# Performance work log

Hardware: AMD Instinct MI355X
Metric: run time of the kernel (lower is better)

The kernel has to match this reference:

```python
import jax, jax.numpy as jnp
import numpy as np


def setup_inputs() -> dict:
    key = jax.random.key(0)
    k1, k2, k3 = jax.random.split(key, 3)
    B, S_enc, S_dec, D = 8, 4096, 4096, 128
    b = jax.random.normal(k1, (B, S_enc, D), dtype=jnp.float32)
    h = jax.random.normal(k2, (B, S_dec, D), dtype=jnp.float32)
    W_b = jax.random.normal(k3, (D, D), dtype=jnp.float32) * (1.0 / np.sqrt(D))
    return {"b": b, "h": h, "W_b": W_b}


def reference(b, h, W_b):
    # tmp1 = h @ W_b : [B, S_dec, D]
    tmp1 = jnp.einsum('btd,de->bte', h, W_b)
    # scores = tmp1 @ b^T : [B, S_dec, S_enc]
    scores = jnp.einsum('bte,bse->bts', tmp1, b)
    attn = jax.nn.softmax(scores, axis=-1)
    # weighted sum over encoder positions (the original does this via a huge
    # tile/broadcast/multiply/reduce_sum; math is a batched matmul)
    cxt = jnp.einsum('bts,bsd->btd', attn, b)
    return cxt
```

## Files before the change

kernel.cpp:

```cpp
#include <hip/hip_runtime.h>

typedef _Float16 half2v __attribute__((ext_vector_type(2)));
typedef _Float16 half4 __attribute__((ext_vector_type(4)));
typedef _Float16 half8 __attribute__((ext_vector_type(8)));
typedef float floatx4 __attribute__((ext_vector_type(4)));

#define B_   8
#define SE   4096
#define SD   4096
#define D_   128
#define NT   64
#define LDB  136
#define LOG2E 1.44269504f

__device__ __forceinline__ void cp16_async(const _Float16* g, _Float16* l) {
    __builtin_amdgcn_global_load_lds((const __attribute__((address_space(1))) unsigned int*)g,
                                     (__attribute__((address_space(3))) unsigned int*)l, 16, 0, 0);
}

__device__ __forceinline__ float dot2acc(half2v a, half2v b, float c) {
#if __has_builtin(__builtin_amdgcn_fdot2)
    return __builtin_amdgcn_fdot2(a, b, c, false);
#else
    return c + (float)a[0] * (float)b[0] + (float)a[1] * (float)b[1];
#endif
}

__global__ __launch_bounds__(256) void wprep(const float* __restrict__ W,
                                             _Float16* __restrict__ W16,
                                             _Float16* __restrict__ Wlo) {
    int i = blockIdx.x * 256 + threadIdx.x;
    float w = W[i];
    _Float16 hi = (_Float16)w;
    W16[i] = hi;
    Wlo[i] = (_Float16)(w - (float)hi);
}

__global__ __launch_bounds__(256) void kvprep(const float* __restrict__ b,
                                              const _Float16* __restrict__ W16,
                                              const _Float16* __restrict__ Wlo,
                                              _Float16* __restrict__ kp,
                                              _Float16* __restrict__ vT) {
    __shared__ _Float16 bs[64 * LDB];
    const int bb = blockIdx.y, s0 = blockIdx.x * 64;
    const int tid = threadIdx.x, wave = tid >> 6, lane = tid & 63;
    const int l15 = lane & 15, quad = lane >> 4;

    const float* bg = b + ((size_t)bb * SE + s0) * D_;
    #pragma unroll
    for (int it = 0; it < 4; ++it) {
        int idx = tid + it * 256;
        int row = idx >> 4, seg = idx & 15;
        const float* src = bg + row * D_ + seg * 8;
        float4 a = *(const float4*)src;
        float4 c = *(const float4*)(src + 4);
        half8 hv;
        hv[0] = (_Float16)a.x; hv[1] = (_Float16)a.y; hv[2] = (_Float16)a.z; hv[3] = (_Float16)a.w;
        hv[4] = (_Float16)c.x; hv[5] = (_Float16)c.y; hv[6] = (_Float16)c.z; hv[7] = (_Float16)c.w;
        *(half8*)(bs + row * LDB + seg * 8) = hv;
    }
    __syncthreads();

    half8 af[4];
    #pragma unroll
    for (int ks = 0; ks < 4; ++ks)
        af[ks] = *(const half8*)(bs + (wave * 16 + l15) * LDB + ks * 32 + quad * 8);
    floatx4 acc[8];
    #pragma unroll
    for (int nt = 0; nt < 8; ++nt) acc[nt] = (floatx4){0.f, 0.f, 0.f, 0.f};
    #pragma unroll
    for (int ks = 0; ks < 4; ++ks) {
        #pragma unroll
        for (int nt = 0; nt < 8; ++nt) {
            half8 bh = *(const half8*)(W16 + (size_t)(nt * 16 + l15) * 128 + ks * 32 + quad * 8);
            half8 bl = *(const half8*)(Wlo + (size_t)(nt * 16 + l15) * 128 + ks * 32 + quad * 8);
            acc[nt] = __builtin_amdgcn_mfma_f32_16x16x32_f16(af[ks], bh, acc[nt], 0, 0, 0);
            acc[nt] = __builtin_amdgcn_mfma_f32_16x16x32_f16(af[ks], bl, acc[nt], 0, 0, 0);
        }
    }

    {
        const int sq = tid & 15, dg = tid >> 4;
        half8 rowv[4];
        #pragma unroll
        for (int j = 0; j < 4; ++j)
            rowv[j] = *(const half8*)(bs + (sq * 4 + j) * LDB + dg * 8);
        #pragma unroll
        for (int r = 0; r < 8; ++r) {
            int d = dg * 8 + r;
            half4 o;
            #pragma unroll
            for (int j = 0; j < 4; ++j) o[j] = rowv[j][r];
            *(half4*)(vT + ((size_t)bb * D_ + d) * SE + s0 + sq * 4) = o;
        }
    }
    __syncthreads();

    #pragma unroll
    for (int nt = 0; nt < 8; ++nt)
        #pragma unroll
        for (int r = 0; r < 4; ++r)
            bs[(wave * 16 + quad * 4 + r) * LDB + nt * 16 + l15] = (_Float16)acc[nt][r];
    __syncthreads();
    _Float16* kg = kp + ((size_t)bb * SE + s0) * D_;
    {
        const int row = tid >> 2;
        #pragma unroll
        for (int it = 0; it < 4; ++it) {
            int ch = (tid & 3) + it * 4;
            half8 v = *(const half8*)(bs + row * LDB + ch * 8);
            *(half8*)(kg + row * D_ + ch * 8) = v;
        }
    }
}

__global__ __launch_bounds__(512, 4) void flash(const float* __restrict__ h,
                                                const _Float16* __restrict__ k,
                                                const _Float16* __restrict__ vT,
                                                float* __restrict__ out) {
    __shared__ _Float16 KV[2][16384];

    const int bb   = blockIdx.y;
    const int q0   = blockIdx.x * 64;
    const int tid  = threadIdx.x;
    const int wave = tid >> 6;
    const int wq   = wave >> 1;
    const int ws   = wave & 1;
    const int lane = tid & 63;
    const int l15  = lane & 15;
    const int quad = lane >> 4;

    const _Float16* kbase = k + (size_t)bb * SE * D_;
    const _Float16* vbase = vT + (size_t)bb * D_ * SE;

    int koff[2], voff[2];
    #pragma unroll
    for (int it = 0; it < 2; ++it) {
        int i = it * 512 + wave * 64 + lane;
        int kr = i >> 4, kpp = i & 15;
        int km = kr & 15;
        int srow = (kr & 32) + ((km >> 2) << 3) + (((kr >> 4) & 1) << 2) + (km & 3);
        koff[it] = srow * D_ + ((kpp ^ km) * 8);
        int vr = i >> 3, vpp = i & 7;
        voff[it] = vr * SE + ((vpp ^ (vr & 7)) * 8);
    }

    const _Float16* kA0[4]; const _Float16* kA1[4];
    const _Float16 *vB0, *vB1;
    #pragma unroll
    for (int ks = 0; ks < 4; ++ks) {
        int o = l15 * 128 + (((ks * 4 + quad) ^ l15) * 8) + ws * 4096;
        kA0[ks] = &KV[0][o]; kA1[ks] = &KV[1][o];
    }
    {
        int o = 8192 + l15 * 64 + (((ws * 4 + quad) ^ (l15 & 7)) * 8);
        vB0 = &KV[0][o]; vB1 = &KV[1][o];
    }

    {
        _Float16* buf0 = &KV[0][0];
        #pragma unroll
        for (int it = 0; it < 2; ++it) {
            cp16_async(kbase + koff[it], buf0 + (it * 512 + wave * 64) * 8);
            cp16_async(vbase + voff[it], buf0 + 8192 + (it * 512 + wave * 64) * 8);
        }
    }

    half8 qf[4];
    {
        const float* hrow = h + ((size_t)bb * SD + q0 + wq * 16 + l15) * D_;
        #pragma unroll
        for (int ks = 0; ks < 4; ++ks) {
            float4 a = *(const float4*)(hrow + ks * 32 + quad * 8);
            float4 c = *(const float4*)(hrow + ks * 32 + quad * 8 + 4);
            half8 f;
            f[0] = (_Float16)(a.x * LOG2E); f[1] = (_Float16)(a.y * LOG2E);
            f[2] = (_Float16)(a.z * LOG2E); f[3] = (_Float16)(a.w * LOG2E);
            f[4] = (_Float16)(c.x * LOG2E); f[5] = (_Float16)(c.y * LOG2E);
            f[6] = (_Float16)(c.z * LOG2E); f[7] = (_Float16)(c.w * LOG2E);
            qf[ks] = f;
        }
    }

    floatx4 acc_o[8];
    #pragma unroll
    for (int dt = 0; dt < 8; ++dt) acc_o[dt] = (floatx4){0.f, 0.f, 0.f, 0.f};
    float nm = 0.f;
    float l_part = 0.f;
    const half2v one2 = { (_Float16)1.f, (_Float16)1.f };

#define STEP(T, KA, VBP, NBUF)                                                        \
  {                                                                                   \
    __syncthreads();                  \
    if ((T) + 1 < SE / NT) {                                                          \
      const _Float16* kt = kbase + (size_t)((T) + 1) * (NT * D_);                     \
      const _Float16* vt = vbase + (size_t)((T) + 1) * NT;                            \
      _Float16* bufn = (NBUF);                                                        \
      _Pragma("unroll")                                                               \
      for (int it = 0; it < 2; ++it) {                                                \
        cp16_async(kt + koff[it], bufn + (it * 512 + wave * 64) * 8);                 \
        cp16_async(vt + voff[it], bufn + 8192 + (it * 512 + wave * 64) * 8);          \
      }                                                                               \
    }                                                                                 \
                        \
    floatx4 accs[2];                                                                  \
    accs[0] = (floatx4){nm, nm, nm, nm};                                              \
    accs[1] = accs[0];                                                                \
    _Pragma("unroll")                                                                 \
    for (int ks = 0; ks < 4; ++ks) {                                                  \
      half8 af0 = *(const half8*)(KA[ks]);                                            \
      half8 af1 = *(const half8*)(KA[ks] + 2048);                                     \
      accs[0] = __builtin_amdgcn_mfma_f32_16x16x32_f16(af0, qf[ks], accs[0], 0, 0, 0);\
      accs[1] = __builtin_amdgcn_mfma_f32_16x16x32_f16(af1, qf[ks], accs[1], 0, 0, 0);\
    }                                                                                 \
                                     \
    float x0 = fmaxf(fmaxf(accs[0][0], accs[0][1]), accs[0][2]);                      \
    float x1 = fmaxf(fmaxf(accs[0][3], accs[1][0]), accs[1][1]);                      \
    float x2 = fmaxf(fmaxf(accs[1][2], accs[1][3]), x0);                              \
    float mv = fmaxf(x1, x2);                                                         \
    if (__ballot(mv > 11.5f) != 0ull) {              \
      float mr = fmaxf(mv, __shfl_xor(mv, 16, 64));                                   \
      mr = fmaxf(mr, __shfl_xor(mr, 32, 64));                                         \
      float delta = fmaxf(mr, 0.f);                                                   \
      float alpha = exp2f(-delta);                                                    \
      l_part *= alpha;                                                                \
      float ab[4];                                                                    \
      _Pragma("unroll")                                                               \
      for (int r = 0; r < 4; ++r) ab[r] = __shfl(alpha, quad * 4 + r, 64);            \
      _Pragma("unroll")                                                               \
      for (int dt = 0; dt < 8; ++dt)                                                  \
        _Pragma("unroll")                                                             \
        for (int r = 0; r < 4; ++r) acc_o[dt][r] *= ab[r];                            \
      _Pragma("unroll")                                                               \
      for (int stl = 0; stl < 2; ++stl)                                               \
        _Pragma("unroll")                                                             \
        for (int r = 0; r < 4; ++r) accs[stl][r] -= delta;                            \
      nm -= delta;                                                                    \
    }                                                                                 \
         \
    float p0 = exp2f(accs[0][0]), p1 = exp2f(accs[0][1]);                             \
    float p2 = exp2f(accs[0][2]), p3 = exp2f(accs[0][3]);                             \
    float p4 = exp2f(accs[1][0]), p5 = exp2f(accs[1][1]);                             \
    float p6 = exp2f(accs[1][2]), p7 = exp2f(accs[1][3]);                             \
    half2v c0 = __builtin_bit_cast(half2v, __builtin_amdgcn_cvt_pkrtz(p0, p1));       \
    half2v c1 = __builtin_bit_cast(half2v, __builtin_amdgcn_cvt_pkrtz(p2, p3));       \
    half2v c2 = __builtin_bit_cast(half2v, __builtin_amdgcn_cvt_pkrtz(p4, p5));       \
    half2v c3 = __builtin_bit_cast(half2v, __builtin_amdgcn_cvt_pkrtz(p6, p7));       \
    l_part = dot2acc(c0, one2, l_part);                                               \
    l_part = dot2acc(c1, one2, l_part);                                               \
    l_part = dot2acc(c2, one2, l_part);                                               \
    l_part = dot2acc(c3, one2, l_part);                                               \
    half8 pA;                                                                         \
    pA[0] = c0[0]; pA[1] = c0[1]; pA[2] = c1[0]; pA[3] = c1[1];                       \
    pA[4] = c2[0]; pA[5] = c2[1]; pA[6] = c3[0]; pA[7] = c3[1];                       \
         \
    _Pragma("unroll")                                                                 \
    for (int dt = 0; dt < 8; ++dt) {                                                  \
      half8 vf = *(const half8*)((VBP) + dt * 1024);                                  \
      acc_o[dt] = __builtin_amdgcn_mfma_f32_16x16x32_f16(pA, vf, acc_o[dt], 0, 0, 0); \
    }                                                                                 \
  }

    for (int t = 0; t < SE / NT; t += 2) {
        STEP(t,     kA0, vB0, &KV[1][0]);
        STEP(t + 1, kA1, vB1, &KV[0][0]);
    }
#undef STEP

    const float m_q = -nm;
    float l_own;
    {
        float l = l_part;
        l += __shfl_xor(l, 16, 64);
        l += __shfl_xor(l, 32, 64);
        l_own = l;
    }

    __syncthreads();
    float* Ob = (float*)&KV[0][0];
    float* ml = (float*)&KV[1][0];

    if (ws == 1) {
        #pragma unroll
        for (int dt = 0; dt < 8; ++dt)
            *(floatx4*)(Ob + ((wq * 8 + dt) * 64 + lane) * 4) = acc_o[dt];
        if (quad == 0)
            *(float2*)(ml + (wq * 16 + l15) * 2) = make_float2(m_q, l_own);
    }
    __syncthreads();
    if (ws == 0) {
        float m0r[4], l0r[4], m1r[4], l1r[4];
        #pragma unroll
        for (int r = 0; r < 4; ++r) {
            m0r[r] = __shfl(m_q, quad * 4 + r, 64);
            l0r[r] = __shfl(l_own, quad * 4 + r, 64);
            float2 p = *(float2*)(ml + (wq * 16 + quad * 4 + r) * 2);
            m1r[r] = p.x; l1r[r] = p.y;
        }
        float a0[4], a1[4], inv[4];
        #pragma unroll
        for (int r = 0; r < 4; ++r) {
            float mm = fmaxf(m0r[r], m1r[r]);
            a0[r] = exp2f(m0r[r] - mm);
            a1[r] = exp2f(m1r[r] - mm);
            inv[r] = 1.f / (l0r[r] * a0[r] + l1r[r] * a1[r]);
        }
        float* orow = out + ((size_t)bb * SD + q0 + wq * 16 + quad * 4) * D_;
        #pragma unroll
        for (int dt = 0; dt < 8; ++dt) {
            floatx4 o1 = *(floatx4*)(Ob + ((wq * 8 + dt) * 64 + lane) * 4);
            #pragma unroll
            for (int r = 0; r < 4; ++r)
                orow[(size_t)r * D_ + dt * 16 + l15] =
                    (acc_o[dt][r] * a0[r] + o1[r] * a1[r]) * inv[r];
        }
    }
}

extern "C" void kernel_launch(void* const* d_in, const int* in_sizes, int n_in,
                              void* d_out, int out_size, void* d_ws, size_t ws_size,
                              hipStream_t stream) {
    const float* b = (const float*)d_in[0];
    const float* h = (const float*)d_in[1];
    const float* W = (const float*)d_in[2];
    float* out = (float*)d_out;

    _Float16* W16 = (_Float16*)d_ws;
    _Float16* Wlo = W16 + 128 * 128;
    _Float16* kp  = Wlo + 128 * 128;
    _Float16* vT  = kp + (size_t)B_ * SE * D_;

    wprep<<<64, 256, 0, stream>>>(W, W16, Wlo);
    kvprep<<<dim3(SE / 64, B_), 256, 0, stream>>>(b, W16, Wlo, kp, vT);
    flash<<<dim3(SD / 64, B_), 512, 0, stream>>>(h, kp, vT, out);
}
```

Baseline: 191.0 us.

## Project queries by W inside flash kernel and give each wave two query tiles

The W projection moves off the keys (b·Wᵀ in a prep kernel) and onto the queries (h·W, computed in the flash kernel's prologue with a transposed split hi/lo W). The prep kernel now only converts b to fp16 and writes its transpose for V. The flash kernel drops to 256 threads, and each wave handles two 16-row query tiles, so every K/V fragment read from LDS feeds twice as many MFMAs. The cost is more accumulator registers per wave, lower occupancy at launch bounds (256,2), and the projection work added to every flash block's prologue.

```diff
diff --git a/kernel.cpp b/kernel.cpp
--- a/kernel.cpp
+++ b/kernel.cpp
@@ -27,26 +27,25 @@
 }
 
 __global__ __launch_bounds__(256) void wprep(const float* __restrict__ W,
-                                             _Float16* __restrict__ W16,
-                                             _Float16* __restrict__ Wlo) {
+                                             _Float16* __restrict__ Wt16,
+                                             _Float16* __restrict__ Wtlo) {
     int i = blockIdx.x * 256 + threadIdx.x;
+    int d = i >> 7, e = i & 127;
     float w = W[i];
     _Float16 hi = (_Float16)w;
-    W16[i] = hi;
-    Wlo[i] = (_Float16)(w - (float)hi);
-}
-
-__global__ __launch_bounds__(256) void kvprep(const float* __restrict__ b,
-                                              const _Float16* __restrict__ W16,
-                                              const _Float16* __restrict__ Wlo,
-                                              _Float16* __restrict__ kp,
-                                              _Float16* __restrict__ vT) {
+    Wt16[e * 128 + d] = hi;
+    Wtlo[e * 128 + d] = (_Float16)(w - (float)hi);
+}
+
+__global__ __launch_bounds__(256) void bprep(const float* __restrict__ b,
+                                             _Float16* __restrict__ kc,
+                                             _Float16* __restrict__ vT) {
     __shared__ _Float16 bs[64 * LDB];
     const int bb = blockIdx.y, s0 = blockIdx.x * 64;
-    const int tid = threadIdx.x, wave = tid >> 6, lane = tid & 63;
-    const int l15 = lane & 15, quad = lane >> 4;
+    const int tid = threadIdx.x;
 
     const float* bg = b + ((size_t)bb * SE + s0) * D_;
+    _Float16* kg = kc + ((size_t)bb * SE + s0) * D_;
     #pragma unroll
     for (int it = 0; it < 4; ++it) {
         int idx = tid + it * 256;
@@ -57,65 +56,29 @@
         half8 hv;
         hv[0] = (_Float16)a.x; hv[1] = (_Float16)a.y; hv[2] = (_Float16)a.z; hv[3] = (_Float16)a.w;
         hv[4] = (_Float16)c.x; hv[5] = (_Float16)c.y; hv[6] = (_Float16)c.z; hv[7] = (_Float16)c.w;
+        *(half8*)(kg + row * D_ + seg * 8) = hv;
         *(half8*)(bs + row * LDB + seg * 8) = hv;
     }
     __syncthreads();
 
-    half8 af[4];
-    #pragma unroll
-    for (int ks = 0; ks < 4; ++ks)
-        af[ks] = *(const half8*)(bs + (wave * 16 + l15) * LDB + ks * 32 + quad * 8);
-    floatx4 acc[8];
-    #pragma unroll
-    for (int nt = 0; nt < 8; ++nt) acc[nt] = (floatx4){0.f, 0.f, 0.f, 0.f};
-    #pragma unroll
-    for (int ks = 0; ks < 4; ++ks) {
-        #pragma unroll
-        for (int nt = 0; nt < 8; ++nt) {
-            half8 bh = *(const half8*)(W16 + (size_t)(nt * 16 + l15) * 128 + ks * 32 + quad * 8);
-            half8 bl = *(const half8*)(Wlo + (size_t)(nt * 16 + l15) * 128 + ks * 32 + quad * 8);
-            acc[nt] = __builtin_amdgcn_mfma_f32_16x16x32_f16(af[ks], bh, acc[nt], 0, 0, 0);
-            acc[nt] = __builtin_amdgcn_mfma_f32_16x16x32_f16(af[ks], bl, acc[nt], 0, 0, 0);
-        }
-    }
-
-    {
-        const int sq = tid & 15, dg = tid >> 4;
-        half8 rowv[4];
-        #pragma unroll
-        for (int j = 0; j < 4; ++j)
-            rowv[j] = *(const half8*)(bs + (sq * 4 + j) * LDB + dg * 8);
-        #pragma unroll
-        for (int r = 0; r < 8; ++r) {
-            int d = dg * 8 + r;
-            half4 o;
-            #pragma unroll
-            for (int j = 0; j < 4; ++j) o[j] = rowv[j][r];
-            *(half4*)(vT + ((size_t)bb * D_ + d) * SE + s0 + sq * 4) = o;
-        }
-    }
-    __syncthreads();
-
-    #pragma unroll
-    for (int nt = 0; nt < 8; ++nt)
-        #pragma unroll
-        for (int r = 0; r < 4; ++r)
-            bs[(wave * 16 + quad * 4 + r) * LDB + nt * 16 + l15] = (_Float16)acc[nt][r];
-    __syncthreads();
-    _Float16* kg = kp + ((size_t)bb * SE + s0) * D_;
-    {
-        const int row = tid >> 2;
-        #pragma unroll
-        for (int it = 0; it < 4; ++it) {
-            int ch = (tid & 3) + it * 4;
-            half8 v = *(const half8*)(bs + row * LDB + ch * 8);
-            *(half8*)(kg + row * D_ + ch * 8) = v;
-        }
-    }
-}
-
-__global__ __launch_bounds__(512, 4) void flash(const float* __restrict__ h,
-                                                const _Float16* __restrict__ k,
+    const int sg = tid & 7, dg = tid >> 3;
+    half4 rowv[8];
+    #pragma unroll
+    for (int j = 0; j < 8; ++j)
+        rowv[j] = *(const half4*)(bs + (sg * 8 + j) * LDB + dg * 4);
+    #pragma unroll
+    for (int dd = 0; dd < 4; ++dd) {
+        half8 o;
+        #pragma unroll
+        for (int j = 0; j < 8; ++j) o[j] = rowv[j][dd];
+        *(half8*)(vT + ((size_t)bb * D_ + dg * 4 + dd) * SE + s0 + sg * 8) = o;
+    }
+}
+
+__global__ __launch_bounds__(256, 2) void flash(const float* __restrict__ h,
+                                                const _Float16* __restrict__ Wt16,
+                                                const _Float16* __restrict__ Wtlo,
+                                                const _Float16* __restrict__ kc,
                                                 const _Float16* __restrict__ vT,
                                                 float* __restrict__ out) {
     __shared__ _Float16 KV[2][16384];
@@ -130,13 +93,13 @@
     const int l15  = lane & 15;
     const int quad = lane >> 4;
 
-    const _Float16* kbase = k + (size_t)bb * SE * D_;
+    const _Float16* kbase = kc + (size_t)bb * SE * D_;
     const _Float16* vbase = vT + (size_t)bb * D_ * SE;
 
-    int koff[2], voff[2];
-    #pragma unroll
-    for (int it = 0; it < 2; ++it) {
-        int i = it * 512 + wave * 64 + lane;
+    int koff[4], voff[4];
+    #pragma unroll
+    for (int it = 0; it < 4; ++it) {
+        int i = it * 256 + wave * 64 + lane;
         int kr = i >> 4, kpp = i & 15;
         int km = kr & 15;
         int srow = (kr & 32) + ((km >> 2) << 3) + (((kr >> 4) & 1) << 2) + (km & 3);
@@ -160,34 +123,107 @@
     {
         _Float16* buf0 = &KV[0][0];
         #pragma unroll
-        for (int it = 0; it < 2; ++it) {
-            cp16_async(kbase + koff[it], buf0 + (it * 512 + wave * 64) * 8);
-            cp16_async(vbase + voff[it], buf0 + 8192 + (it * 512 + wave * 64) * 8);
-        }
-    }
-
-    half8 qf[4];
-    {
-        const float* hrow = h + ((size_t)bb * SD + q0 + wq * 16 + l15) * D_;
+        for (int it = 0; it < 4; ++it) {
+            cp16_async(kbase + koff[it], buf0 + (it * 256 + wave * 64) * 8);
+            cp16_async(vbase + voff[it], buf0 + 8192 + (it * 256 + wave * 64) * 8);
+        }
+    }
+
+    _Float16* hs = &KV[1][0];
+    {
+        const float* hg = h + ((size_t)bb * SD + q0) * D_;
+        #pragma unroll
+        for (int it = 0; it < 4; ++it) {
+            int idx = tid + it * 256;
+            int row = idx >> 4, seg = idx & 15;
+            const float* src = hg + row * D_ + seg * 8;
+            float4 a = *(const float4*)src;
+            float4 c = *(const float4*)(src + 4);
+            half8 hv;
+            hv[0] = (_Float16)a.x; hv[1] = (_Float16)a.y; hv[2] = (_Float16)a.z; hv[3] = (_Float16)a.w;
+            hv[4] = (_Float16)c.x; hv[5] = (_Float16)c.y; hv[6] = (_Float16)c.z; hv[7] = (_Float16)c.w;
+            *(half8*)(hs + row * LDB + seg * 8) = hv;
+        }
+    }
+    __syncthreads();
+    half8 qf0[4], qf1[4];
+    {
+        half8 af[4];
+        #pragma unroll
+        for (int ks = 0; ks < 4; ++ks)
+            af[ks] = *(const half8*)(hs + (wave * 16 + l15) * LDB + ks * 32 + quad * 8);
+        floatx4 acc[8];
+        #pragma unroll
+        for (int nt = 0; nt < 8; ++nt) acc[nt] = (floatx4){0.f, 0.f, 0.f, 0.f};
         #pragma unroll
         for (int ks = 0; ks < 4; ++ks) {
-            float4 a = *(const float4*)(hrow + ks * 32 + quad * 8);
-            float4 c = *(const float4*)(hrow + ks * 32 + quad * 8 + 4);
-            half8 f;
-            f[0] = (_Float16)(a.x * LOG2E); f[1] = (_Float16)(a.y * LOG2E);
-            f[2] = (_Float16)(a.z * LOG2E); f[3] = (_Float16)(a.w * LOG2E);
-            f[4] = (_Float16)(c.x * LOG2E); f[5] = (_Float16)(c.y * LOG2E);
-            f[6] = (_Float16)(c.z * LOG2E); f[7] = (_Float16)(c.w * LOG2E);
-            qf[ks] = f;
-        }
-    }
-
-    floatx4 acc_o[8];
-    #pragma unroll
-    for (int dt = 0; dt < 8; ++dt) acc_o[dt] = (floatx4){0.f, 0.f, 0.f, 0.f};
-    float nm = 0.f;
-    float l_part = 0.f;
+            #pragma unroll
+            for (int nt = 0; nt < 8; ++nt) {
+                half8 bh = *(const half8*)(Wt16 + (size_t)(nt * 16 + l15) * 128 + ks * 32 + quad * 8);
+                half8 bl = *(const half8*)(Wtlo + (size_t)(nt * 16 + l15) * 128 + ks * 32 + quad * 8);
+                acc[nt] = __builtin_amdgcn_mfma_f32_16x16x32_f16(af[ks], bh, acc[nt], 0, 0, 0);
+                acc[nt] = __builtin_amdgcn_mfma_f32_16x16x32_f16(af[ks], bl, acc[nt], 0, 0, 0);
+            }
+        }
+        __syncthreads();
+        #pragma unroll
+        for (int nt = 0; nt < 8; ++nt)
+            #pragma unroll
+            for (int r = 0; r < 4; ++r)
+                hs[(wave * 16 + quad * 4 + r) * LDB + nt * 16 + l15] =
+                    (_Float16)(acc[nt][r] * LOG2E);
+        __syncthreads();
+        #pragma unroll
+        for (int ks = 0; ks < 4; ++ks) {
+            qf0[ks] = *(const half8*)(hs + (wq * 32 + l15) * LDB + ks * 32 + quad * 8);
+            qf1[ks] = *(const half8*)(hs + (wq * 32 + 16 + l15) * LDB + ks * 32 + quad * 8);
+        }
+    }
+
+    floatx4 acc_o0[8], acc_o1[8];
+    #pragma unroll
+    for (int dt = 0; dt < 8; ++dt) {
+        acc_o0[dt] = (floatx4){0.f, 0.f, 0.f, 0.f};
+        acc_o1[dt] = (floatx4){0.f, 0.f, 0.f, 0.f};
+    }
+    float nm0 = 0.f, nm1 = 0.f;
+    float lp0 = 0.f, lp1 = 0.f;
     const half2v one2 = { (_Float16)1.f, (_Float16)1.f };
+
+#define RESCALE(MV, NM, LP, ACCS, ACCO)                                               \
+    { float mr = fmaxf((MV), __shfl_xor((MV), 16, 64));                               \
+      mr = fmaxf(mr, __shfl_xor(mr, 32, 64));                                         \
+      float delta = fmaxf(mr, 0.f);                                                   \
+      float alpha = exp2f(-delta);                                                    \
+      LP *= alpha;                                                                    \
+      float ab[4];                                                                    \
+      _Pragma("unroll")                                                               \
+      for (int r = 0; r < 4; ++r) ab[r] = __shfl(alpha, quad * 4 + r, 64);            \
+      _Pragma("unroll")                                                               \
+      for (int dt = 0; dt < 8; ++dt)                                                  \
+        _Pragma("unroll")                                                             \
+        for (int r = 0; r < 4; ++r) ACCO[dt][r] *= ab[r];                             \
+      _Pragma("unroll")                                                               \
+      for (int stl = 0; stl < 2; ++stl)                                               \
+        _Pragma("unroll")                                                             \
+        for (int r = 0; r < 4; ++r) ACCS[stl][r] -= delta;                            \
+      NM -= delta; }
+
+#define SOFTPACK(ACCS, LP, PA)                                                        \
+    { float p0 = exp2f(ACCS[0][0]), p1 = exp2f(ACCS[0][1]);                           \
+      float p2 = exp2f(ACCS[0][2]), p3 = exp2f(ACCS[0][3]);                           \
+      float p4 = exp2f(ACCS[1][0]), p5 = exp2f(ACCS[1][1]);                           \
+      float p6 = exp2f(ACCS[1][2]), p7 = exp2f(ACCS[1][3]);                           \
+      half2v c0 = __builtin_bit_cast(half2v, __builtin_amdgcn_cvt_pkrtz(p0, p1));     \
+      half2v c1 = __builtin_bit_cast(half2v, __builtin_amdgcn_cvt_pkrtz(p2, p3));     \
+      half2v c2 = __builtin_bit_cast(half2v, __builtin_amdgcn_cvt_pkrtz(p4, p5));     \
+      half2v c3 = __builtin_bit_cast(half2v, __builtin_amdgcn_cvt_pkrtz(p6, p7));     \
+      LP = dot2acc(c0, one2, LP);                                                     \
+      LP = dot2acc(c1, one2, LP);                                                     \
+      LP = dot2acc(c2, one2, LP);                                                     \
+      LP = dot2acc(c3, one2, LP);                                                     \
+      PA[0] = c0[0]; PA[1] = c0[1]; PA[2] = c1[0]; PA[3] = c1[1];                     \
+      PA[4] = c2[0]; PA[5] = c2[1]; PA[6] = c3[0]; PA[7] = c3[1]; }
 
 #define STEP(T, KA, VBP, NBUF)                                                        \
   {                                                                                   \
@@ -197,67 +233,39 @@
       const _Float16* vt = vbase + (size_t)((T) + 1) * NT;                            \
       _Float16* bufn = (NBUF);                                                        \
       _Pragma("unroll")                                                               \
-      for (int it = 0; it < 2; ++it) {                                                \
-        cp16_async(kt + koff[it], bufn + (it * 512 + wave * 64) * 8);                 \
-        cp16_async(vt + voff[it], bufn + 8192 + (it * 512 + wave * 64) * 8);          \
+      for (int it = 0; it < 4; ++it) {                                                \
+        cp16_async(kt + koff[it], bufn + (it * 256 + wave * 64) * 8);                 \
+        cp16_async(vt + voff[it], bufn + 8192 + (it * 256 + wave * 64) * 8);          \
       }                                                                               \
     }                                                                                 \
-                        \
-    floatx4 accs[2];                                                                  \
-    accs[0] = (floatx4){nm, nm, nm, nm};                                              \
-    accs[1] = accs[0];                                                                \
+    floatx4 accs0[2], accs1[2];                                                       \
+    accs0[0] = (floatx4){nm0, nm0, nm0, nm0}; accs0[1] = accs0[0];                    \
+    accs1[0] = (floatx4){nm1, nm1, nm1, nm1}; accs1[1] = accs1[0];                    \
     _Pragma("unroll")                                                                 \
     for (int ks = 0; ks < 4; ++ks) {                                                  \
       half8 af0 = *(const half8*)(KA[ks]);                                            \
       half8 af1 = *(const half8*)(KA[ks] + 2048);                                     \
-      accs[0] = __builtin_amdgcn_mfma_f32_16x16x32_f16(af0, qf[ks], accs[0], 0, 0, 0);\
-      accs[1] = __builtin_amdgcn_mfma_f32_16x16x32_f16(af1, qf[ks], accs[1], 0, 0, 0);\
+      accs0[0] = __builtin_amdgcn_mfma_f32_16x16x32_f16(af0, qf0[ks], accs0[0], 0, 0, 0); \
+      accs0[1] = __builtin_amdgcn_mfma_f32_16x16x32_f16(af1, qf0[ks], accs0[1], 0, 0, 0); \
+      accs1[0] = __builtin_amdgcn_mfma_f32_16x16x32_f16(af0, qf1[ks], accs1[0], 0, 0, 0); \
+      accs1[1] = __builtin_amdgcn_mfma_f32_16x16x32_f16(af1, qf1[ks], accs1[1], 0, 0, 0); \
     }                                                                                 \
-                                     \
-    float x0 = fmaxf(fmaxf(accs[0][0], accs[0][1]), accs[0][2]);                      \
-    float x1 = fmaxf(fmaxf(accs[0][3], accs[1][0]), accs[1][1]);                      \
-    float x2 = fmaxf(fmaxf(accs[1][2], accs[1][3]), x0);                              \
-    float mv = fmaxf(x1, x2);                                                         \
-    if (__ballot(mv > 11.5f) != 0ull) {              \
-      float mr = fmaxf(mv, __shfl_xor(mv, 16, 64));                                   \
-      mr = fmaxf(mr, __shfl_xor(mr, 32, 64));                                         \
-      float delta = fmaxf(mr, 0.f);                                                   \
-      float alpha = exp2f(-delta);                                                    \
-      l_part *= alpha;                                                                \
-      float ab[4];                                                                    \
-      _Pragma("unroll")                                                               \
-      for (int r = 0; r < 4; ++r) ab[r] = __shfl(alpha, quad * 4 + r, 64);            \
-      _Pragma("unroll")                                                               \
-      for (int dt = 0; dt < 8; ++dt)                                                  \
-        _Pragma("unroll")                                                             \
-        for (int r = 0; r < 4; ++r) acc_o[dt][r] *= ab[r];                            \
-      _Pragma("unroll")                                                               \
-      for (int stl = 0; stl < 2; ++stl)                                               \
-        _Pragma("unroll")                                                             \
-        for (int r = 0; r < 4; ++r) accs[stl][r] -= delta;                            \
-      nm -= delta;                                                                    \
+    float mv0 = fmaxf(fmaxf(fmaxf(accs0[0][0], accs0[0][1]), fmaxf(accs0[0][2], accs0[0][3])), \
+                      fmaxf(fmaxf(accs0[1][0], accs0[1][1]), fmaxf(accs0[1][2], accs0[1][3]))); \
+    float mv1 = fmaxf(fmaxf(fmaxf(accs1[0][0], accs1[0][1]), fmaxf(accs1[0][2], accs1[0][3])), \
+                      fmaxf(fmaxf(accs1[1][0], accs1[1][1]), fmaxf(accs1[1][2], accs1[1][3]))); \
+    if (__ballot((mv0 > 11.5f) || (mv1 > 11.5f)) != 0ull) {                           \
+      RESCALE(mv0, nm0, lp0, accs0, acc_o0);                                          \
+      RESCALE(mv1, nm1, lp1, accs1, acc_o1);                                          \
     }                                                                                 \
-         \
-    float p0 = exp2f(accs[0][0]), p1 = exp2f(accs[0][1]);                             \
-    float p2 = exp2f(accs[0][2]), p3 = exp2f(accs[0][3]);                             \
-    float p4 = exp2f(accs[1][0]), p5 = exp2f(accs[1][1]);                             \
-    float p6 = exp2f(accs[1][2]), p7 = exp2f(accs[1][3]);                             \
-    half2v c0 = __builtin_bit_cast(half2v, __builtin_amdgcn_cvt_pkrtz(p0, p1));       \
-    half2v c1 = __builtin_bit_cast(half2v, __builtin_amdgcn_cvt_pkrtz(p2, p3));       \
-    half2v c2 = __builtin_bit_cast(half2v, __builtin_amdgcn_cvt_pkrtz(p4, p5));       \
-    half2v c3 = __builtin_bit_cast(half2v, __builtin_amdgcn_cvt_pkrtz(p6, p7));       \
-    l_part = dot2acc(c0, one2, l_part);                                               \
-    l_part = dot2acc(c1, one2, l_part);                                               \
-    l_part = dot2acc(c2, one2, l_part);                                               \
-    l_part = dot2acc(c3, one2, l_part);                                               \
-    half8 pA;                                                                         \
-    pA[0] = c0[0]; pA[1] = c0[1]; pA[2] = c1[0]; pA[3] = c1[1];                       \
-    pA[4] = c2[0]; pA[5] = c2[1]; pA[6] = c3[0]; pA[7] = c3[1];                       \
-         \
+    half8 pA0, pA1;                                                                   \
+    SOFTPACK(accs0, lp0, pA0);                                                        \
+    SOFTPACK(accs1, lp1, pA1);                                                        \
     _Pragma("unroll")                                                                 \
     for (int dt = 0; dt < 8; ++dt) {                                                  \
       half8 vf = *(const half8*)((VBP) + dt * 1024);                                  \
-      acc_o[dt] = __builtin_amdgcn_mfma_f32_16x16x32_f16(pA, vf, acc_o[dt], 0, 0, 0); \
+      acc_o0[dt] = __builtin_amdgcn_mfma_f32_16x16x32_f16(pA0, vf, acc_o0[dt], 0, 0, 0); \
+      acc_o1[dt] = __builtin_amdgcn_mfma_f32_16x16x32_f16(pA1, vf, acc_o1[dt], 0, 0, 0); \
     }                                                                                 \
   }
 
@@ -267,13 +275,17 @@
     }
 #undef STEP
 
-    const float m_q = -nm;
-    float l_own;
-    {
-        float l = l_part;
+    const float m_q0 = -nm0, m_q1 = -nm1;
+    float lo0, lo1;
+    {
+        float l = lp0;
         l += __shfl_xor(l, 16, 64);
         l += __shfl_xor(l, 32, 64);
-        l_own = l;
+        lo0 = l;
+        l = lp1;
+        l += __shfl_xor(l, 16, 64);
+        l += __shfl_xor(l, 32, 64);
+        lo1 = l;
     }
 
     __syncthreads();
@@ -282,39 +294,49 @@
 
     if (ws == 1) {
         #pragma unroll
-        for (int dt = 0; dt < 8; ++dt)
-            *(floatx4*)(Ob + ((wq * 8 + dt) * 64 + lane) * 4) = acc_o[dt];
-        if (quad == 0)
-            *(float2*)(ml + (wq * 16 + l15) * 2) = make_float2(m_q, l_own);
+        for (int dt = 0; dt < 8; ++dt) {
+            *(floatx4*)(Ob + (((wq * 2 + 0) * 8 + dt) * 64 + lane) * 4) = acc_o0[dt];
+            *(floatx4*)(Ob + (((wq * 2 + 1) * 8 + dt) * 64 + lane) * 4) = acc_o1[dt];
+        }
+        if (quad == 0) {
+            *(float2*)(ml + (wq * 32 + l15) * 2)      = make_float2(m_q0, lo0);
+            *(float2*)(ml + (wq * 32 + 16 + l15) * 2) = make_float2(m_q1, lo1);
+        }
     }
     __syncthreads();
     if (ws == 0) {
-        float m0r[4], l0r[4], m1r[4], l1r[4];
-        #pragma unroll
-        for (int r = 0; r < 4; ++r) {
-            m0r[r] = __shfl(m_q, quad * 4 + r, 64);
-            l0r[r] = __shfl(l_own, quad * 4 + r, 64);
-            float2 p = *(float2*)(ml + (wq * 16 + quad * 4 + r) * 2);
-            m1r[r] = p.x; l1r[r] = p.y;
-        }
-        float a0[4], a1[4], inv[4];
-        #pragma unroll
-        for (int r = 0; r < 4; ++r) {
-            float mm = fmaxf(m0r[r], m1r[r]);
-            a0[r] = exp2f(m0r[r] - mm);
-            a1[r] = exp2f(m1r[r] - mm);
-            inv[r] = 1.f / (l0r[r] * a0[r] + l1r[r] * a1[r]);
-        }
-        float* orow = out + ((size_t)bb * SD + q0 + wq * 16 + quad * 4) * D_;
-        #pragma unroll
-        for (int dt = 0; dt < 8; ++dt) {
-            floatx4 o1 = *(floatx4*)(Ob + ((wq * 8 + dt) * 64 + lane) * 4);
-            #pragma unroll
-            for (int r = 0; r < 4; ++r)
-                orow[(size_t)r * D_ + dt * 16 + l15] =
-                    (acc_o[dt][r] * a0[r] + o1[r] * a1[r]) * inv[r];
-        }
-    }
+#define MERGE(ACC, MQ, LO, QQ)                                                        \
+      { float m0r[4], l0r[4], m1r[4], l1r[4];                                         \
+        _Pragma("unroll")                                                             \
+        for (int r = 0; r < 4; ++r) {                                                 \
+            m0r[r] = __shfl((MQ), quad * 4 + r, 64);                                  \
+            l0r[r] = __shfl((LO), quad * 4 + r, 64);                                  \
+            float2 p = *(float2*)(ml + (wq * 32 + (QQ) * 16 + quad * 4 + r) * 2);     \
+            m1r[r] = p.x; l1r[r] = p.y;                                               \
+        }                                                                             \
+        float a0[4], a1[4], inv[4];                                                   \
+        _Pragma("unroll")                                                             \
+        for (int r = 0; r < 4; ++r) {                                                 \
+            float mm = fmaxf(m0r[r], m1r[r]);                                         \
+            a0[r] = exp2f(m0r[r] - mm);                                               \
+            a1[r] = exp2f(m1r[r] - mm);                                               \
+            inv[r] = 1.f / (l0r[r] * a0[r] + l1r[r] * a1[r]);                         \
+        }                                                                             \
+        float* orow = out + ((size_t)bb * SD + q0 + wq * 32 + (QQ) * 16 + quad * 4) * D_; \
+        _Pragma("unroll")                                                             \
+        for (int dt = 0; dt < 8; ++dt) {                                              \
+            floatx4 o1 = *(floatx4*)(Ob + (((wq * 2 + (QQ)) * 8 + dt) * 64 + lane) * 4); \
+            _Pragma("unroll")                                                         \
+            for (int r = 0; r < 4; ++r)                                               \
+                orow[(size_t)r * D_ + dt * 16 + l15] =                                \
+                    (ACC[dt][r] * a0[r] + o1[r] * a1[r]) * inv[r];                    \
+        } }
+        MERGE(acc_o0, m_q0, lo0, 0);
+        MERGE(acc_o1, m_q1, lo1, 1);
+#undef MERGE
+    }
+#undef RESCALE
+#undef SOFTPACK
 }
 
 extern "C" void kernel_launch(void* const* d_in, const int* in_sizes, int n_in,
@@ -325,12 +347,12 @@
     const float* W = (const float*)d_in[2];
     float* out = (float*)d_out;
 
-    _Float16* W16 = (_Float16*)d_ws;
-    _Float16* Wlo = W16 + 128 * 128;
-    _Float16* kp  = Wlo + 128 * 128;
-    _Float16* vT  = kp + (size_t)B_ * SE * D_;
-
-    wprep<<<64, 256, 0, stream>>>(W, W16, Wlo);
-    kvprep<<<dim3(SE / 64, B_), 256, 0, stream>>>(b, W16, Wlo, kp, vT);
-    flash<<<dim3(SD / 64, B_), 512, 0, stream>>>(h, kp, vT, out);
-}
+    _Float16* Wt16 = (_Float16*)d_ws;
+    _Float16* Wtlo = Wt16 + 128 * 128;
+    _Float16* kc   = Wtlo + 128 * 128;
+    _Float16* vT   = kc + (size_t)B_ * SE * D_;
+
+    wprep<<<64, 256, 0, stream>>>(W, Wt16, Wtlo);
+    bprep<<<dim3(SE / 64, B_), 256, 0, stream>>>(b, kc, vT);
+    flash<<<dim3(SD / 64, B_), 256, 0, stream>>>(h, Wt16, Wtlo, kc, vT, out);
+}
```

Result: slower. 199.3 us (+4.4%).

## Move bilinear projection from encoder keys onto query tiles and fuse weight prep

Applied to the files above, without the earlier changes.

Attention scores are now computed as (h·W)·b^T instead of h·(b·W^T)^T. Each flash block projects its 64 query rows through W using split-fp16 MFMAs, staging them through shared memory, and keys become a plain fp16 copy of b. The separate weight-split kernel is folded into the key/value prep kernel, which removes one launch and the MFMA work from that memory-bound pass. The value transpose now uses wider 16-byte stores. The cost is extra syncs and prologue latency in the flash kernel, plus a different fp16 rounding point (q rounded after projection instead of k).

```diff
diff --git a/kernel.cpp b/kernel.cpp
--- a/kernel.cpp
+++ b/kernel.cpp
@@ -26,27 +26,31 @@
 #endif
 }
 
-__global__ __launch_bounds__(256) void wprep(const float* __restrict__ W,
-                                             _Float16* __restrict__ W16,
-                                             _Float16* __restrict__ Wlo) {
-    int i = blockIdx.x * 256 + threadIdx.x;
-    float w = W[i];
-    _Float16 hi = (_Float16)w;
-    W16[i] = hi;
-    Wlo[i] = (_Float16)(w - (float)hi);
-}
-
-__global__ __launch_bounds__(256) void kvprep(const float* __restrict__ b,
-                                              const _Float16* __restrict__ W16,
-                                              const _Float16* __restrict__ Wlo,
-                                              _Float16* __restrict__ kp,
-                                              _Float16* __restrict__ vT) {
+__global__ __launch_bounds__(256) void bprep(const float* __restrict__ b,
+                                             const float* __restrict__ W,
+                                             _Float16* __restrict__ kc,
+                                             _Float16* __restrict__ vT,
+                                             _Float16* __restrict__ Wt16,
+                                             _Float16* __restrict__ Wtlo) {
     __shared__ _Float16 bs[64 * LDB];
     const int bb = blockIdx.y, s0 = blockIdx.x * 64;
-    const int tid = threadIdx.x, wave = tid >> 6, lane = tid & 63;
-    const int l15 = lane & 15, quad = lane >> 4;
+    const int tid = threadIdx.x;
+
+    if (blockIdx.x == 0) {
+        int base = bb * 2048 + tid * 8;
+        #pragma unroll
+        for (int j = 0; j < 8; ++j) {
+            int i = base + j;
+            int d = i >> 7, e = i & 127;
+            float w = W[i];
+            _Float16 hi = (_Float16)w;
+            Wt16[e * 128 + d] = hi;
+            Wtlo[e * 128 + d] = (_Float16)(w - (float)hi);
+        }
+    }
 
     const float* bg = b + ((size_t)bb * SE + s0) * D_;
+    _Float16* kg = kc + ((size_t)bb * SE + s0) * D_;
     #pragma unroll
     for (int it = 0; it < 4; ++it) {
         int idx = tid + it * 256;
@@ -57,65 +61,29 @@
         half8 hv;
         hv[0] = (_Float16)a.x; hv[1] = (_Float16)a.y; hv[2] = (_Float16)a.z; hv[3] = (_Float16)a.w;
         hv[4] = (_Float16)c.x; hv[5] = (_Float16)c.y; hv[6] = (_Float16)c.z; hv[7] = (_Float16)c.w;
+        *(half8*)(kg + row * D_ + seg * 8) = hv;
         *(half8*)(bs + row * LDB + seg * 8) = hv;
     }
     __syncthreads();
 
-    half8 af[4];
-    #pragma unroll
-    for (int ks = 0; ks < 4; ++ks)
-        af[ks] = *(const half8*)(bs + (wave * 16 + l15) * LDB + ks * 32 + quad * 8);
-    floatx4 acc[8];
-    #pragma unroll
-    for (int nt = 0; nt < 8; ++nt) acc[nt] = (floatx4){0.f, 0.f, 0.f, 0.f};
-    #pragma unroll
-    for (int ks = 0; ks < 4; ++ks) {
-        #pragma unroll
-        for (int nt = 0; nt < 8; ++nt) {
-            half8 bh = *(const half8*)(W16 + (size_t)(nt * 16 + l15) * 128 + ks * 32 + quad * 8);
-            half8 bl = *(const half8*)(Wlo + (size_t)(nt * 16 + l15) * 128 + ks * 32 + quad * 8);
-            acc[nt] = __builtin_amdgcn_mfma_f32_16x16x32_f16(af[ks], bh, acc[nt], 0, 0, 0);
-            acc[nt] = __builtin_amdgcn_mfma_f32_16x16x32_f16(af[ks], bl, acc[nt], 0, 0, 0);
-        }
-    }
-
-    {
-        const int sq = tid & 15, dg = tid >> 4;
-        half8 rowv[4];
-        #pragma unroll
-        for (int j = 0; j < 4; ++j)
-            rowv[j] = *(const half8*)(bs + (sq * 4 + j) * LDB + dg * 8);
-        #pragma unroll
-        for (int r = 0; r < 8; ++r) {
-            int d = dg * 8 + r;
-            half4 o;
-            #pragma unroll
-            for (int j = 0; j < 4; ++j) o[j] = rowv[j][r];
-            *(half4*)(vT + ((size_t)bb * D_ + d) * SE + s0 + sq * 4) = o;
-        }
-    }
-    __syncthreads();
-
-    #pragma unroll
-    for (int nt = 0; nt < 8; ++nt)
-        #pragma unroll
-        for (int r = 0; r < 4; ++r)
-            bs[(wave * 16 + quad * 4 + r) * LDB + nt * 16 + l15] = (_Float16)acc[nt][r];
-    __syncthreads();
-    _Float16* kg = kp + ((size_t)bb * SE + s0) * D_;
-    {
-        const int row = tid >> 2;
-        #pragma unroll
-        for (int it = 0; it < 4; ++it) {
-            int ch = (tid & 3) + it * 4;
-            half8 v = *(const half8*)(bs + row * LDB + ch * 8);
-            *(half8*)(kg + row * D_ + ch * 8) = v;
-        }
+    const int sg = tid & 7, dg = tid >> 3;
+    half4 rowv[8];
+    #pragma unroll
+    for (int j = 0; j < 8; ++j)
+        rowv[j] = *(const half4*)(bs + (sg * 8 + j) * LDB + dg * 4);
+    #pragma unroll
+    for (int dd = 0; dd < 4; ++dd) {
+        half8 o;
+        #pragma unroll
+        for (int j = 0; j < 8; ++j) o[j] = rowv[j][dd];
+        *(half8*)(vT + ((size_t)bb * D_ + dg * 4 + dd) * SE + s0 + sg * 8) = o;
     }
 }
 
 __global__ __launch_bounds__(512, 4) void flash(const float* __restrict__ h,
-                                                const _Float16* __restrict__ k,
+                                                const _Float16* __restrict__ Wt16,
+                                                const _Float16* __restrict__ Wtlo,
+                                                const _Float16* __restrict__ kc,
                                                 const _Float16* __restrict__ vT,
                                                 float* __restrict__ out) {
     __shared__ _Float16 KV[2][16384];
@@ -130,7 +98,7 @@
     const int l15  = lane & 15;
     const int quad = lane >> 4;
 
-    const _Float16* kbase = k + (size_t)bb * SE * D_;
+    const _Float16* kbase = kc + (size_t)bb * SE * D_;
     const _Float16* vbase = vT + (size_t)bb * D_ * SE;
 
     int koff[2], voff[2];
@@ -166,20 +134,54 @@
         }
     }
 
+    _Float16* hs = &KV[1][0];
+    {
+        const float* hg = h + ((size_t)bb * SD + q0) * D_;
+        #pragma unroll
+        for (int it = 0; it < 2; ++it) {
+            int idx = tid + it * 512;
+            int row = idx >> 4, seg = idx & 15;
+            const float* src = hg + row * D_ + seg * 8;
+            float4 a = *(const float4*)src;
+            float4 c = *(const float4*)(src + 4);
+            half8 hv;
+            hv[0] = (_Float16)a.x; hv[1] = (_Float16)a.y; hv[2] = (_Float16)a.z; hv[3] = (_Float16)a.w;
+            hv[4] = (_Float16)c.x; hv[5] = (_Float16)c.y; hv[6] = (_Float16)c.z; hv[7] = (_Float16)c.w;
+            *(half8*)(hs + row * LDB + seg * 8) = hv;
+        }
+    }
+    __syncthreads();
     half8 qf[4];
     {
-        const float* hrow = h + ((size_t)bb * SD + q0 + wq * 16 + l15) * D_;
+        half8 af[4];
+        #pragma unroll
+        for (int ks = 0; ks < 4; ++ks)
+            af[ks] = *(const half8*)(hs + (wq * 16 + l15) * LDB + ks * 32 + quad * 8);
+        floatx4 acc[4];
+        #pragma unroll
+        for (int nt = 0; nt < 4; ++nt) acc[nt] = (floatx4){0.f, 0.f, 0.f, 0.f};
         #pragma unroll
         for (int ks = 0; ks < 4; ++ks) {
-            float4 a = *(const float4*)(hrow + ks * 32 + quad * 8);
-            float4 c = *(const float4*)(hrow + ks * 32 + quad * 8 + 4);
-            half8 f;
-            f[0] = (_Float16)(a.x * LOG2E); f[1] = (_Float16)(a.y * LOG2E);
-            f[2] = (_Float16)(a.z * LOG2E); f[3] = (_Float16)(a.w * LOG2E);
-            f[4] = (_Float16)(c.x * LOG2E); f[5] = (_Float16)(c.y * LOG2E);
-            f[6] = (_Float16)(c.z * LOG2E); f[7] = (_Float16)(c.w * LOG2E);
-            qf[ks] = f;
-        }
+            #pragma unroll
+            for (int nt = 0; nt < 4; ++nt) {
+                size_t wo = (size_t)(ws * 64 + nt * 16 + l15) * 128 + ks * 32 + quad * 8;
+                half8 bh = *(const half8*)(Wt16 + wo);
+                half8 bl = *(const half8*)(Wtlo + wo);
+                acc[nt] = __builtin_amdgcn_mfma_f32_16x16x32_f16(af[ks], bh, acc[nt], 0, 0, 0);
+                acc[nt] = __builtin_amdgcn_mfma_f32_16x16x32_f16(af[ks], bl, acc[nt], 0, 0, 0);
+            }
+        }
+        __syncthreads();
+        #pragma unroll
+        for (int nt = 0; nt < 4; ++nt)
+            #pragma unroll
+            for (int r = 0; r < 4; ++r)
+                hs[(wq * 16 + quad * 4 + r) * LDB + ws * 64 + nt * 16 + l15] =
+                    (_Float16)(acc[nt][r] * LOG2E);
+        __syncthreads();
+        #pragma unroll
+        for (int ks = 0; ks < 4; ++ks)
+            qf[ks] = *(const half8*)(hs + (wq * 16 + l15) * LDB + ks * 32 + quad * 8);
     }
 
     floatx4 acc_o[8];
@@ -325,12 +327,11 @@
     const float* W = (const float*)d_in[2];
     float* out = (float*)d_out;
 
-    _Float16* W16 = (_Float16*)d_ws;
-    _Float16* Wlo = W16 + 128 * 128;
-    _Float16* kp  = Wlo + 128 * 128;
-    _Float16* vT  = kp + (size_t)B_ * SE * D_;
-
-    wprep<<<64, 256, 0, stream>>>(W, W16, Wlo);
-    kvprep<<<dim3(SE / 64, B_), 256, 0, stream>>>(b, W16, Wlo, kp, vT);
-    flash<<<dim3(SD / 64, B_), 512, 0, stream>>>(h, kp, vT, out);
-}
+    _Float16* Wt16 = (_Float16*)d_ws;
+    _Float16* Wtlo = Wt16 + 128 * 128;
+    _Float16* kc   = Wtlo + 128 * 128;
+    _Float16* vT   = kc + (size_t)B_ * SE * D_;
+
+    bprep<<<dim3(SE / 64, B_), 256, 0, stream>>>(b, W, kc, vT, Wt16, Wtlo);
+    flash<<<dim3(SD / 64, B_), 512, 0, stream>>>(h, Wt16, Wtlo, kc, vT, out);
+}
```

Result: faster. 185.1 us (-3.1%).
